# Performance work log

Measured on AMD Instinct MI355X. Metric: run time of the kernel, lower is better.

The kernel has to match this reference:

```python
import jax, jax.numpy as jnp
import numpy as np

D_EMB = 1024
NUM_HEADS = 16
HEAD_DIM = D_EMB // NUM_HEADS
SCALE = HEAD_DIM ** -0.5


def setup_inputs() -> dict:
    key = jax.random.key(0)
    ks = jax.random.split(key, 5)
    B, L = 2, 2048
    x = jax.random.normal(ks[0], (B, L, D_EMB), dtype=jnp.float32)
    # nn.Linear default init scale ~ U(-1/sqrt(fan_in), 1/sqrt(fan_in))
    s = 1.0 / np.sqrt(D_EMB)
    w_qkv = jax.random.uniform(ks[1], (D_EMB, 3 * D_EMB), jnp.float32, -s, s)
    b_qkv = jax.random.uniform(ks[2], (3 * D_EMB,), jnp.float32, -s, s)
    w_proj = jax.random.uniform(ks[3], (D_EMB, D_EMB), jnp.float32, -s, s)
    b_proj = jax.random.uniform(ks[4], (D_EMB,), jnp.float32, -s, s)
    return {"x": x, "w_qkv": w_qkv, "b_qkv": b_qkv, "w_proj": w_proj, "b_proj": b_proj}


def reference(x, w_qkv, b_qkv, w_proj, b_proj):
    B, L, C = x.shape
    qkv = x @ w_qkv + b_qkv                      # [B, L, 3C]
    q, k, v = jnp.split(qkv, 3, axis=-1)
    # [B, L, C] -> [B, H, L, Dh]
    def split_heads(t):
        return t.reshape(B, L, NUM_HEADS, HEAD_DIM).transpose(0, 2, 1, 3)
    q, k, v = split_heads(q), split_heads(k), split_heads(v)
    attn = jnp.einsum("bhqd,bhkd->bhqk", q, k) * SCALE   # [B, H, L, L]
    attn = jax.nn.softmax(attn, axis=-1)
    out = jnp.einsum("bhqk,bhkd->bhqd", attn, v)          # [B, H, L, Dh]
    out = out.transpose(0, 2, 1, 3).reshape(B, L, C)
    return out @ w_proj + b_proj
```

## Files before the change

kernel.cpp:

```cpp
#include <hip/hip_runtime.h>

typedef __attribute__((ext_vector_type(8))) __bf16 bf16x8;
typedef __attribute__((ext_vector_type(4))) __bf16 bf16x4;
typedef __attribute__((ext_vector_type(4))) float f32x4;
typedef __attribute__((ext_vector_type(16))) float f32x16;

#define AS1 __attribute__((address_space(1)))
#define AS3 __attribute__((address_space(3)))

#define QSCALE 0.18033688011112042f

__device__ __forceinline__ void gload_lds16(const void* g, void* l) {
  __builtin_amdgcn_global_load_lds((const AS1 void*)g, (AS3 void*)l, 16, 0, 0);
}

__device__ __forceinline__ float ex2(float x) { return __builtin_amdgcn_exp2f(x); }

__device__ __forceinline__ unsigned pkbf16(float lo, float hi) {
  union { __bf16 h; unsigned short u; } a, b;
  a.h = (__bf16)lo; b.h = (__bf16)hi;
  return (unsigned)a.u | ((unsigned)b.u << 16);
}

__device__ __forceinline__ void pls32(unsigned& a, unsigned& b) {
  asm("v_permlane32_swap_b32 %0, %1" : "+v"(a), "+v"(b));
}

union U8 { unsigned u[4]; bf16x8 v; };


__global__ void cvt_f32_to_bf16(const float* __restrict__ in, __bf16* __restrict__ out, int n4) {
  int i = blockIdx.x * blockDim.x + threadIdx.x;
  int stride = gridDim.x * blockDim.x;
  const float4* in4 = (const float4*)in;
  for (; i < n4; i += stride) {
    float4 v = in4[i];
    bf16x4 o;
    o[0] = (__bf16)v.x; o[1] = (__bf16)v.y; o[2] = (__bf16)v.z; o[3] = (__bf16)v.w;
    *(bf16x4*)(out + 4 * (size_t)i) = o;
  }
}

__global__ void transpose_f32_to_bf16(const float* __restrict__ in, __bf16* __restrict__ out,
                                      int K, int N, int scale_lim, float scale) {
  __shared__ float tile[32][33];
  int tx = threadIdx.x, ty = threadIdx.y;
  int n0 = blockIdx.x * 32, k0 = blockIdx.y * 32;
#pragma unroll
  for (int i = 0; i < 4; i++)
    tile[ty + 8 * i][tx] = in[(size_t)(k0 + ty + 8 * i) * N + n0 + tx];
  __syncthreads();
#pragma unroll
  for (int i = 0; i < 4; i++) {
    int n = n0 + ty + 8 * i;
    float v = tile[tx][ty + 8 * i];
    if (n < scale_lim) v *= scale;
    out[(size_t)n * K + k0 + tx] = (__bf16)v;
  }
}


#define GEMM_MAINLOOP(A, BT, K)                                                        \
  f32x4 acc[4][4] = {};                                                                \
  for (int kt = 0; kt < (K); kt += 64) {                                               \
    _Pragma("unroll") for (int j = 0; j < 4; j++) {                                    \
      int c = j * 256 + t;                                                             \
      int row = c >> 3, kc = c & 7;                                                    \
      gload_lds16((A) + (size_t)(m0 + row) * (K) + kt + ((kc ^ (row & 7)) << 3),       \
                  As + ((j * 256 + w * 64) << 3));                                     \
    }                                                                                  \
    _Pragma("unroll") for (int j = 0; j < 4; j++) {                                    \
      int c = j * 256 + t;                                                             \
      int row = c >> 3, kc = c & 7;                                                    \
      gload_lds16((BT) + (size_t)(n0 + row) * (K) + kt + ((kc ^ (row & 7)) << 3),      \
                  Bs + ((j * 256 + w * 64) << 3));                                     \
    }                                                                                  \
    __syncthreads();                                                                   \
    _Pragma("unroll") for (int ks = 0; ks < 2; ks++) {                                 \
      bf16x8 af[4], bfr[4];                                                            \
      _Pragma("unroll") for (int fm = 0; fm < 4; fm++) {                               \
        int row = wr * 64 + fm * 16 + l15;                                             \
        int off = row * 128 + ((ks * 64 + (lg << 4)) ^ ((row & 7) << 4));              \
        af[fm] = *(const bf16x8*)((const char*)As + off);                              \
      }                                                                                \
      _Pragma("unroll") for (int fn = 0; fn < 4; fn++) {                               \
        int row = wc * 64 + fn * 16 + l15;                                             \
        int off = row * 128 + ((ks * 64 + (lg << 4)) ^ ((row & 7) << 4));              \
        bfr[fn] = *(const bf16x8*)((const char*)Bs + off);                             \
      }                                                                                \
      __builtin_amdgcn_s_setprio(1);                                                   \
      _Pragma("unroll") for (int fm = 0; fm < 4; fm++)                                 \
        _Pragma("unroll") for (int fn = 0; fn < 4; fn++)                               \
          acc[fm][fn] =                                                                \
              __builtin_amdgcn_mfma_f32_16x16x32_bf16(af[fm], bfr[fn], acc[fm][fn], 0, 0, 0); \
      __builtin_amdgcn_s_setprio(0);                                                   \
    }                                                                                  \
    __syncthreads();                                                                   \
  }

__global__ __launch_bounds__(256) void gemm_qkv(
    const __bf16* __restrict__ A, const __bf16* __restrict__ BT,
    const float* __restrict__ bias,
    __bf16* __restrict__ Qb, __bf16* __restrict__ Kb, __bf16* __restrict__ Vtb) {
  __shared__ __align__(16) __bf16 As[128 * 64];
  __shared__ __align__(16) __bf16 Bs[128 * 64];
  const int t = threadIdx.x;
  const int l = t & 63, w = t >> 6;
  const int wr = w >> 1, wc = w & 1;
  const int m0 = blockIdx.y * 128, n0 = blockIdx.x * 128;
  const int l15 = l & 15, lg = l >> 4;

  GEMM_MAINLOOP(A, BT, 1024)

#pragma unroll
  for (int fn = 0; fn < 4; fn++) {
    int n = n0 + wc * 64 + fn * 16 + l15;
    int sec = n >> 10, idx = n & 1023;
    int hh = idx >> 6, d = idx & 63;
    float bv = bias[n];
    if (sec == 0) bv *= QSCALE;
#pragma unroll
    for (int fm = 0; fm < 4; fm++) {
      int mb = m0 + wr * 64 + fm * 16 + (lg << 2);
#pragma unroll
      for (int r = 0; r < 4; r++) {
        int m = mb + r;
        float v = acc[fm][fn][r] + bv;
        size_t bho = (size_t)(((m >> 11) << 4) + hh) * 131072;
        int pos = m & 2047;
        if (sec == 0)
          Qb[bho + (size_t)pos * 64 + d] = (__bf16)v;
        else if (sec == 1)
          Kb[bho + (size_t)pos * 64 + d] = (__bf16)v;
        else
          Vtb[bho + (size_t)d * 2048 + pos] = (__bf16)v;
      }
    }
  }
}

__global__ __launch_bounds__(256) void gemm_proj(
    const __bf16* __restrict__ A, const __bf16* __restrict__ BT,
    const float* __restrict__ bias, float* __restrict__ outf, int N, int K) {
  __shared__ __align__(16) __bf16 As[128 * 64];
  __shared__ __align__(16) __bf16 Bs[128 * 64];
  const int t = threadIdx.x;
  const int l = t & 63, w = t >> 6;
  const int wr = w >> 1, wc = w & 1;
  const int m0 = blockIdx.y * 128, n0 = blockIdx.x * 128;
  const int l15 = l & 15, lg = l >> 4;

  GEMM_MAINLOOP(A, BT, K)

#pragma unroll
  for (int fn = 0; fn < 4; fn++) {
    int n = n0 + wc * 64 + fn * 16 + l15;
    float bv = bias[n];
#pragma unroll
    for (int fm = 0; fm < 4; fm++) {
      int mbase = m0 + wr * 64 + fm * 16 + (lg << 2);
#pragma unroll
      for (int r = 0; r < 4; r++)
        outf[(size_t)(mbase + r) * N + n] = acc[fm][fn][r] + bv;
    }
  }
}


__global__ __launch_bounds__(256, 2) void flash_attn(
    const __bf16* __restrict__ Qb, const __bf16* __restrict__ Kb,
    const __bf16* __restrict__ Vtb, __bf16* __restrict__ o) {
  __shared__ __align__(16) __bf16 Ks[64 * 64];
  __shared__ __align__(16) __bf16 Vt[64 * 64];
  const int t = threadIdx.x;
  const int l = t & 63, w = t >> 6;
  const int l31 = l & 31, hi = l >> 5;
  const int bh = blockIdx.y;
  const int q0 = blockIdx.x * 128 + w * 32;
  const __bf16* kbase = Kb + (size_t)bh * 131072;
  const __bf16* vbase = Vtb + (size_t)bh * 131072;

  bf16x8 qf[4];
#pragma unroll
  for (int kf = 0; kf < 4; kf++)
    qf[kf] = *(const bf16x8*)(Qb + (size_t)bh * 131072 + (size_t)(q0 + l31) * 64 +
                              kf * 16 + hi * 8);

  f32x16 oa0 = {}, oa1 = {};
  float l_run = 0.f;

#define STAGE(ktn)                                                                  \
  _Pragma("unroll") for (int j = 0; j < 2; j++) {                                   \
    int c = j * 256 + t;                                                            \
    int row = c >> 3, kc = c & 7;                                                   \
    gload_lds16(kbase + (size_t)((ktn) + row) * 64 + ((kc ^ (row & 7)) << 3),       \
                (char*)Ks + (j * 256 + w * 64) * 16);                               \
    gload_lds16(vbase + (size_t)row * 2048 + (ktn) + ((kc ^ (row & 7)) << 3),       \
                (char*)Vt + (j * 256 + w * 64) * 16);                               \
  }

  STAGE(0)
  __syncthreads();

  for (int it = 0; it < 32; ++it) {
    bf16x8 kfr0[4], kfr1[4], vfr0[4], vfr1[4];
#pragma unroll
    for (int kf = 0; kf < 4; kf++) {
      int off = (kf * 32 + hi * 16) ^ ((l31 & 7) << 4);
      kfr0[kf] = *(const bf16x8*)((const char*)Ks + l31 * 128 + off);
      kfr1[kf] = *(const bf16x8*)((const char*)Ks + (32 + l31) * 128 + off);
      vfr0[kf] = *(const bf16x8*)((const char*)Vt + l31 * 128 + off);
      vfr1[kf] = *(const bf16x8*)((const char*)Vt + (32 + l31) * 128 + off);
    }
    __syncthreads();

    if (it < 31) { STAGE((it + 1) * 64) }

    f32x16 s0 = {}, s1 = {};
    __builtin_amdgcn_s_setprio(1);
#pragma unroll
    for (int kf = 0; kf < 4; kf++) {
      s0 = __builtin_amdgcn_mfma_f32_32x32x16_bf16(kfr0[kf], qf[kf], s0, 0, 0, 0);
      s1 = __builtin_amdgcn_mfma_f32_32x32x16_bf16(kfr1[kf], qf[kf], s1, 0, 0, 0);
    }
    __builtin_amdgcn_s_setprio(0);

    float sum = 0.f;
#pragma unroll
    for (int r = 0; r < 16; r++) { s0[r] = ex2(s0[r]); sum += s0[r]; }
#pragma unroll
    for (int r = 0; r < 16; r++) { s1[r] = ex2(s1[r]); sum += s1[r]; }
    sum += __shfl_xor(sum, 32);
    l_run += sum;

    unsigned wk0[8], wk1[8];
#pragma unroll
    for (int j = 0; j < 8; j++) wk0[j] = pkbf16(s0[2 * j], s0[2 * j + 1]);
#pragma unroll
    for (int j = 0; j < 8; j++) wk1[j] = pkbf16(s1[2 * j], s1[2 * j + 1]);

    U8 pa[4];
    {
      unsigned a0 = wk0[0], b0 = wk0[2], a1 = wk0[1], b1 = wk0[3];
      pls32(a0, b0); pls32(a1, b1);
      pa[0].u[0] = a0; pa[0].u[1] = a1; pa[0].u[2] = b0; pa[0].u[3] = b1;
      unsigned a2 = wk0[4], b2 = wk0[6], a3 = wk0[5], b3 = wk0[7];
      pls32(a2, b2); pls32(a3, b3);
      pa[1].u[0] = a2; pa[1].u[1] = a3; pa[1].u[2] = b2; pa[1].u[3] = b3;
      unsigned a4 = wk1[0], b4 = wk1[2], a5 = wk1[1], b5 = wk1[3];
      pls32(a4, b4); pls32(a5, b5);
      pa[2].u[0] = a4; pa[2].u[1] = a5; pa[2].u[2] = b4; pa[2].u[3] = b5;
      unsigned a6 = wk1[4], b6 = wk1[6], a7 = wk1[5], b7 = wk1[7];
      pls32(a6, b6); pls32(a7, b7);
      pa[3].u[0] = a6; pa[3].u[1] = a7; pa[3].u[2] = b6; pa[3].u[3] = b7;
    }

    __builtin_amdgcn_s_setprio(1);
#pragma unroll
    for (int ks = 0; ks < 4; ks++) {
      oa0 = __builtin_amdgcn_mfma_f32_32x32x16_bf16(pa[ks].v, vfr0[ks], oa0, 0, 0, 0);
      oa1 = __builtin_amdgcn_mfma_f32_32x32x16_bf16(pa[ks].v, vfr1[ks], oa1, 0, 0, 0);
    }
    __builtin_amdgcn_s_setprio(0);

    __syncthreads();
  }

  float inv = 1.0f / l_run;
  const int b = bh >> 4, h = bh & 15;
#pragma unroll
  for (int r = 0; r < 16; ++r) {
    int crow = (r & 3) + ((r >> 2) << 3) + (hi << 2);
    float ir = __shfl(inv, crow);
    size_t grow = (size_t)(b * 2048 + q0 + crow);
    o[grow * 1024 + h * 64 + l31] = (__bf16)(oa0[r] * ir);
    o[grow * 1024 + h * 64 + 32 + l31] = (__bf16)(oa1[r] * ir);
  }
}


extern "C" void kernel_launch(void* const* d_in, const int* in_sizes, int n_in,
                              void* d_out, int out_size, void* d_ws, size_t ws_size,
                              hipStream_t stream) {
  const float* x      = (const float*)d_in[0];
  const float* w_qkv  = (const float*)d_in[1];
  const float* b_qkv  = (const float*)d_in[2];
  const float* w_proj = (const float*)d_in[3];
  const float* b_proj = (const float*)d_in[4];
  float* out = (float*)d_out;

  char* ws = (char*)d_ws;
  __bf16* xb     = (__bf16*)(ws);
  __bf16* wqkvT  = (__bf16*)(ws + 8388608);
  __bf16* wprojT = (__bf16*)(ws + 14680064);
  __bf16* Qb     = (__bf16*)(ws + 16777216);
  __bf16* Kb     = (__bf16*)(ws + 25165824);
  __bf16* Vtb    = (__bf16*)(ws + 33554432);
  __bf16* attno  = (__bf16*)(ws + 41943040);

  cvt_f32_to_bf16<<<2048, 256, 0, stream>>>(x, xb, 4096 * 1024 / 4);
  transpose_f32_to_bf16<<<dim3(96, 32), dim3(32, 8), 0, stream>>>(w_qkv, wqkvT, 1024, 3072,
                                                                  1024, QSCALE);
  transpose_f32_to_bf16<<<dim3(32, 32), dim3(32, 8), 0, stream>>>(w_proj, wprojT, 1024, 1024,
                                                                  0, 1.0f);
  gemm_qkv<<<dim3(24, 32), 256, 0, stream>>>(xb, wqkvT, b_qkv, Qb, Kb, Vtb);
  flash_attn<<<dim3(16, 32), 256, 0, stream>>>(Qb, Kb, Vtb, attno);
  gemm_proj<<<dim3(8, 32), 256, 0, stream>>>(attno, wprojT, b_proj, out, 1024, 1024);
}
```

Before: 215.4 us.

## Write V row-major in QKV GEMM, transpose separately, halve proj GEMM N-tile

```diff
diff --git a/kernel.cpp b/kernel.cpp
--- a/kernel.cpp
+++ b/kernel.cpp
@@ -57,6 +57,21 @@
     if (n < scale_lim) v *= scale;
     out[(size_t)n * K + k0 + tx] = (__bf16)v;
   }
+}
+
+__global__ void transpose_v(const __bf16* __restrict__ in, __bf16* __restrict__ out) {
+  __shared__ __bf16 tile[32][33];
+  int tx = threadIdx.x, ty = threadIdx.y;
+  int p0 = blockIdx.x * 32, d0 = blockIdx.y * 32;
+  const __bf16* src = in + (size_t)blockIdx.z * 131072;
+  __bf16* dst = out + (size_t)blockIdx.z * 131072;
+#pragma unroll
+  for (int i = 0; i < 4; i++)
+    tile[ty + 8 * i][tx] = src[(size_t)(p0 + ty + 8 * i) * 64 + d0 + tx];
+  __syncthreads();
+#pragma unroll
+  for (int i = 0; i < 4; i++)
+    dst[(size_t)(d0 + ty + 8 * i) * 2048 + p0 + tx] = tile[tx][ty + 8 * i];
 }
 
 
@@ -101,7 +116,7 @@
 __global__ __launch_bounds__(256) void gemm_qkv(
     const __bf16* __restrict__ A, const __bf16* __restrict__ BT,
     const float* __restrict__ bias,
-    __bf16* __restrict__ Qb, __bf16* __restrict__ Kb, __bf16* __restrict__ Vtb) {
+    __bf16* __restrict__ Qb, __bf16* __restrict__ Kb, __bf16* __restrict__ Vb) {
   __shared__ __align__(16) __bf16 As[128 * 64];
   __shared__ __align__(16) __bf16 Bs[128 * 64];
   const int t = threadIdx.x;
@@ -119,21 +134,15 @@
     int hh = idx >> 6, d = idx & 63;
     float bv = bias[n];
     if (sec == 0) bv *= QSCALE;
+    __bf16* dst = sec == 0 ? Qb : (sec == 1 ? Kb : Vb);
 #pragma unroll
     for (int fm = 0; fm < 4; fm++) {
       int mb = m0 + wr * 64 + fm * 16 + (lg << 2);
 #pragma unroll
       for (int r = 0; r < 4; r++) {
         int m = mb + r;
-        float v = acc[fm][fn][r] + bv;
-        size_t bho = (size_t)(((m >> 11) << 4) + hh) * 131072;
-        int pos = m & 2047;
-        if (sec == 0)
-          Qb[bho + (size_t)pos * 64 + d] = (__bf16)v;
-        else if (sec == 1)
-          Kb[bho + (size_t)pos * 64 + d] = (__bf16)v;
-        else
-          Vtb[bho + (size_t)d * 2048 + pos] = (__bf16)v;
+        dst[(size_t)(((m >> 11) << 4) + hh) * 131072 + (size_t)(m & 2047) * 64 + d] =
+            (__bf16)(acc[fm][fn][r] + bv);
       }
     }
   }
@@ -141,27 +150,68 @@
 
 __global__ __launch_bounds__(256) void gemm_proj(
     const __bf16* __restrict__ A, const __bf16* __restrict__ BT,
-    const float* __restrict__ bias, float* __restrict__ outf, int N, int K) {
+    const float* __restrict__ bias, float* __restrict__ outf) {
   __shared__ __align__(16) __bf16 As[128 * 64];
-  __shared__ __align__(16) __bf16 Bs[128 * 64];
+  __shared__ __align__(16) __bf16 Bs[64 * 64];
   const int t = threadIdx.x;
   const int l = t & 63, w = t >> 6;
   const int wr = w >> 1, wc = w & 1;
-  const int m0 = blockIdx.y * 128, n0 = blockIdx.x * 128;
+  const int m0 = blockIdx.y * 128, n0 = blockIdx.x * 64;
   const int l15 = l & 15, lg = l >> 4;
 
-  GEMM_MAINLOOP(A, BT, K)
-
-#pragma unroll
-  for (int fn = 0; fn < 4; fn++) {
-    int n = n0 + wc * 64 + fn * 16 + l15;
+  f32x4 acc[4][2] = {};
+  for (int kt = 0; kt < 1024; kt += 64) {
+#pragma unroll
+    for (int j = 0; j < 4; j++) {
+      int c = j * 256 + t;
+      int row = c >> 3, kc = c & 7;
+      gload_lds16(A + (size_t)(m0 + row) * 1024 + kt + ((kc ^ (row & 7)) << 3),
+                  As + ((j * 256 + w * 64) << 3));
+    }
+#pragma unroll
+    for (int j = 0; j < 2; j++) {
+      int c = j * 256 + t;
+      int row = c >> 3, kc = c & 7;
+      gload_lds16(BT + (size_t)(n0 + row) * 1024 + kt + ((kc ^ (row & 7)) << 3),
+                  Bs + ((j * 256 + w * 64) << 3));
+    }
+    __syncthreads();
+#pragma unroll
+    for (int ks = 0; ks < 2; ks++) {
+      bf16x8 af[4], bfr[2];
+#pragma unroll
+      for (int fm = 0; fm < 4; fm++) {
+        int row = wr * 64 + fm * 16 + l15;
+        int off = row * 128 + ((ks * 64 + (lg << 4)) ^ ((row & 7) << 4));
+        af[fm] = *(const bf16x8*)((const char*)As + off);
+      }
+#pragma unroll
+      for (int fn = 0; fn < 2; fn++) {
+        int row = wc * 32 + fn * 16 + l15;
+        int off = row * 128 + ((ks * 64 + (lg << 4)) ^ ((row & 7) << 4));
+        bfr[fn] = *(const bf16x8*)((const char*)Bs + off);
+      }
+      __builtin_amdgcn_s_setprio(1);
+#pragma unroll
+      for (int fm = 0; fm < 4; fm++)
+#pragma unroll
+        for (int fn = 0; fn < 2; fn++)
+          acc[fm][fn] = __builtin_amdgcn_mfma_f32_16x16x32_bf16(af[fm], bfr[fn], acc[fm][fn], 0, 0, 0);
+      __builtin_amdgcn_s_setprio(0);
+    }
+    __syncthreads();
+  }
+
+#pragma unroll
+  for (int fn = 0; fn < 2; fn++) {
+    int n = n0 + wc * 32 + fn * 16 + l15;
     float bv = bias[n];
 #pragma unroll
     for (int fm = 0; fm < 4; fm++) {
       int mbase = m0 + wr * 64 + fm * 16 + (lg << 2);
 #pragma unroll
       for (int r = 0; r < 4; r++)
-        outf[(size_t)(mbase + r) * N + n] = acc[fm][fn][r] + bv;
+        outf[(size_t)(mbase + r) * 1024 + n] = acc[fm][fn][r] + bv;
     }
   }
 }
@@ -291,11 +341,12 @@
 
   char* ws = (char*)d_ws;
   __bf16* xb     = (__bf16*)(ws);
+  __bf16* Vtb    = (__bf16*)(ws);
   __bf16* wqkvT  = (__bf16*)(ws + 8388608);
   __bf16* wprojT = (__bf16*)(ws + 14680064);
   __bf16* Qb     = (__bf16*)(ws + 16777216);
   __bf16* Kb     = (__bf16*)(ws + 25165824);
-  __bf16* Vtb    = (__bf16*)(ws + 33554432);
+  __bf16* Vb     = (__bf16*)(ws + 33554432);
   __bf16* attno  = (__bf16*)(ws + 41943040);
 
   cvt_f32_to_bf16<<<2048, 256, 0, stream>>>(x, xb, 4096 * 1024 / 4);
@@ -303,7 +354,8 @@
                                                                   1024, QSCALE);
   transpose_f32_to_bf16<<<dim3(32, 32), dim3(32, 8), 0, stream>>>(w_proj, wprojT, 1024, 1024,
                                                                   0, 1.0f);
-  gemm_qkv<<<dim3(24, 32), 256, 0, stream>>>(xb, wqkvT, b_qkv, Qb, Kb, Vtb);
+  gemm_qkv<<<dim3(24, 32), 256, 0, stream>>>(xb, wqkvT, b_qkv, Qb, Kb, Vb);
+  transpose_v<<<dim3(64, 2, 32), dim3(32, 8), 0, stream>>>(Vb, Vtb);
   flash_attn<<<dim3(16, 32), 256, 0, stream>>>(Qb, Kb, Vtb, attno);
-  gemm_proj<<<dim3(8, 32), 256, 0, stream>>>(attno, wprojT, b_proj, out, 1024, 1024);
-}
+  gemm_proj<<<dim3(16, 32), 256, 0, stream>>>(attno, wprojT, b_proj, out);
+}
```

After: 196.3 us. 1.1x faster.
